# Performance work log

Measured on AMD Instinct MI355X. Metric: run time of the kernel, lower is better.

Reference implementation:

```python
import jax, jax.numpy as jnp
import numpy as np

DIM = 128      # transformer_dim = bottleneck_ch
NHEADS = 4
NEXP = 16
EHID = 256
WS = 8         # window_size
EPS = 1e-5     # LayerNorm eps


def setup_inputs() -> dict:
    key = jax.random.key(0)
    ks = jax.random.split(key, 6)
    B, H, W = 2, 128, 128
    N = H * W
    s = 0.02
    return {
        "x": jax.random.normal(ks[0], (B, N, DIM), jnp.float32),
        "ln1_g": jnp.ones((DIM,), jnp.float32),
        "ln1_b": jnp.zeros((DIM,), jnp.float32),
        "w_qkv": jax.random.normal(ks[1], (3 * DIM, DIM), jnp.float32) * s,
        "b_qkv": jnp.zeros((3 * DIM,), jnp.float32),
        "w_proj": jax.random.normal(ks[2], (DIM, DIM), jnp.float32) * s,
        "b_proj": jnp.zeros((DIM,), jnp.float32),
        "ln2_g": jnp.ones((DIM,), jnp.float32),
        "ln2_b": jnp.zeros((DIM,), jnp.float32),
        "gate_w": jax.random.normal(ks[3], (NEXP, DIM), jnp.float32) * s,
        "w1": jax.random.normal(ks[4], (NEXP, EHID, DIM), jnp.float32) * s,
        "b1": jnp.zeros((NEXP, EHID), jnp.float32),
        "w2": jax.random.normal(ks[5], (NEXP, DIM, EHID), jnp.float32) * s,
        "b2": jnp.zeros((NEXP, DIM), jnp.float32),
        "H": H,
        "W": W,
    }


def _ln(x, g, b):
    m = jnp.mean(x, axis=-1, keepdims=True)
    v = jnp.var(x, axis=-1, keepdims=True)
    return (x - m) * jax.lax.rsqrt(v + EPS) * g + b


def _win_attn(x, H, W, w_qkv, b_qkv, w_proj, b_proj):
    # x: (B, N, C); H,W divisible by WS (no padding branch needed)
    B, N, C = x.shape
    hd = C // NHEADS
    nH, nW = H // WS, W // WS
    # window partition: (B, N, C) -> (B*nH*nW, WS*WS, C)
    xw = x.reshape(B, nH, WS, nW, WS, C).transpose(0, 1, 3, 2, 4, 5)
    xw = xw.reshape(B * nH * nW, WS * WS, C)
    qkv = xw @ w_qkv.T + b_qkv
    q, k, v = jnp.split(qkv, 3, axis=-1)
    def heads(t):
        return t.reshape(-1, WS * WS, NHEADS, hd).transpose(0, 2, 1, 3)
    q, k, v = heads(q), heads(k), heads(v)
    scores = jnp.einsum('whqd,whkd->whqk', q, k) / jnp.sqrt(jnp.float32(hd))
    a = jax.nn.softmax(scores, axis=-1)
    o = jnp.einsum('whqk,whkd->whqd', a, v).transpose(0, 2, 1, 3)
    o = o.reshape(-1, WS * WS, C) @ w_proj.T + b_proj
    # window merge back to (B, N, C)
    o = o.reshape(B, nH, nW, WS, WS, C).transpose(0, 1, 3, 2, 4, 5)
    return o.reshape(B, N, C)


def _moe(x, gate_w, w1, b1, w2, b2):
    # top_k = 1 routing, eval mode (no noise / aux losses)
    B, N, C = x.shape
    f = x.reshape(-1, C)                      # (T, C)
    logits = f @ gate_w.T                     # (T, E)
    probs = jax.nn.softmax(logits, axis=-1)
    p = jnp.max(probs, axis=-1)               # top-1 prob
    idx = jnp.argmax(probs, axis=-1)          # top-1 expert id
    wgt = p / (p + 1e-8)                      # top_k_probs / (sum + eps)
    out = jnp.zeros_like(f)
    for e in range(NEXP):                     # small fixed expert loop
        h = jax.nn.gelu(f @ w1[e].T + b1[e], approximate=False)
        eo = h @ w2[e].T + b2[e]
        out = out + jnp.where((idx == e)[:, None], eo, 0.0)
    return (out * wgt[:, None]).reshape(B, N, C)


def reference(x, ln1_g, ln1_b, w_qkv, b_qkv, w_proj, b_proj,
              ln2_g, ln2_b, gate_w, w1, b1, w2, b2, H, W):
    x = x + _win_attn(_ln(x, ln1_g, ln1_b), H, W, w_qkv, b_qkv, w_proj, b_proj)
    x = x + _moe(_ln(x, ln2_g, ln2_b), gate_w, w1, b1, w2, b2)
    return x
```

## Files before the change

### kernel.cpp

```cpp
#include <hip/hip_runtime.h>
#include <math.h>

#define T_TOK 32768
#define DIM 128
#define NHEADS 4
#define HD 32
#define NEXP 16
#define EHID 256
#define NWIN 512
#define EPS 1e-5f
#define CPAD 16
#define XFS 132

typedef _Float16 f16x8 __attribute__((ext_vector_type(8)));
typedef _Float16 f16x4 __attribute__((ext_vector_type(4)));
typedef float f32x4v __attribute__((ext_vector_type(4)));

#define MFMA16(a, b, c) __builtin_amdgcn_mfma_f32_16x16x32_f16(a, b, c, 0, 0, 0)
#define LO_SCALE 4096.0f
#define LO_INV (1.0f / 4096.0f)

__device__ __forceinline__ int sw128(int r, int c) {
    return r * 128 + (((c >> 3) ^ (r & 7)) << 3) + (c & 7);
}
__device__ __forceinline__ int sw64(int r, int c) {
    return r * 64 + (((c >> 3) ^ (r & 7)) << 3) + (c & 7);
}
__device__ __forceinline__ int sw64p(int r, int c) {
    return r * 64 + (((c >> 3) ^ ((r ^ (r >> 3)) & 7)) << 3) + (c & 7);
}
__device__ __forceinline__ int swht(int tok, int hid) {
    return tok * 256 + (((hid >> 3) ^ (tok & 7)) << 3) + (hid & 7);
}

__global__ __launch_bounds__(256) void k_cvt(
    const float* __restrict__ wqkv, const float* __restrict__ wproj,
    _Float16* __restrict__ wq_h, _Float16* __restrict__ wq_l,
    _Float16* __restrict__ wp_h, _Float16* __restrict__ wp_l,
    int* __restrict__ counts)
{
    int i = blockIdx.x * 256 + threadIdx.x;
    if (blockIdx.x == 0 && threadIdx.x < NEXP * CPAD) counts[threadIdx.x] = 0;
    if (i < 3 * DIM * DIM / 4) {
        float4 f = ((const float4*)wqkv)[i];
        float fv[4] = {f.x, f.y, f.z, f.w};
        f16x4 h, l;
        #pragma unroll
        for (int j = 0; j < 4; ++j) {
            _Float16 hh = (_Float16)fv[j];
            h[j] = hh;
            l[j] = (_Float16)((fv[j] - (float)hh) * LO_SCALE);
        }
        *(f16x4*)(wq_h + (size_t)i * 4) = h;
        *(f16x4*)(wq_l + (size_t)i * 4) = l;
    }
    if (i < DIM * DIM / 4) {
        float4 f = ((const float4*)wproj)[i];
        float fv[4] = {f.x, f.y, f.z, f.w};
        f16x4 h, l;
        #pragma unroll
        for (int j = 0; j < 4; ++j) {
            _Float16 hh = (_Float16)fv[j];
            h[j] = hh;
            l[j] = (_Float16)((fv[j] - (float)hh) * LO_SCALE);
        }
        *(f16x4*)(wp_h + (size_t)i * 4) = h;
        *(f16x4*)(wp_l + (size_t)i * 4) = l;
    }
}

__global__ __launch_bounds__(1024) void k_attn(
    const float* __restrict__ x,
    const float* __restrict__ ln_g, const float* __restrict__ ln_b,
    const _Float16* __restrict__ wq_h, const _Float16* __restrict__ wq_l,
    const float* __restrict__ b_qkv,
    const _Float16* __restrict__ wp_h, const _Float16* __restrict__ wp_l,
    const float* __restrict__ b_proj,
    const float* __restrict__ ln2_g, const float* __restrict__ ln2_b,
    const float* __restrict__ gw,
    const float* __restrict__ w1, const float* __restrict__ w2,
    _Float16* __restrict__ w1h, _Float16* __restrict__ w2h,
    float* __restrict__ x2, _Float16* __restrict__ y2,
    float* __restrict__ wgt, int* __restrict__ perm, int* __restrict__ counts)
{
    __shared__ __align__(16) char smem[131072];
    _Float16* xoh = (_Float16*)(smem);
    _Float16* xol = (_Float16*)(smem + 16384);
    _Float16* qh  = (_Float16*)(smem + 32768);
    _Float16* ql  = (_Float16*)(smem + 49152);
    _Float16* kh  = (_Float16*)(smem + 65536);
    _Float16* kl  = (_Float16*)(smem + 81920);
    _Float16* vth = (_Float16*)(smem + 98304);
    _Float16* vtl = (_Float16*)(smem + 114688);
    float* xf   = (float*)(smem + 32768);
    float* ylds = (float*)(smem + 66560);
    float* lgs  = (float*)(smem + 99584);

    int tid = threadIdx.x;
    int w = tid >> 6, lane = tid & 63;
    int l15 = lane & 15, lg = lane >> 4;
    int wid = blockIdx.x;
    int wb = wid >> 8, wrr = (wid >> 4) & 15, wcc = wid & 15;
    const int tokbase = wb * 16384 + wrr * 1024 + wcc * 8;
    const size_t base = (size_t)tokbase * DIM;

    f16x8 qbh[2][4], qbl[2][4];
    float qbias[2];
    #pragma unroll
    for (int tl = 0; tl < 2; ++tl) {
        if (tl == 1 && w >= 8) break;
        int o = ((tl == 0) ? w : 16 + w) * 16 + l15;
        qbias[tl] = b_qkv[o];
        #pragma unroll
        for (int ks = 0; ks < 4; ++ks) {
            size_t wo = (size_t)o * DIM + ks * 32 + lg * 8;
            qbh[tl][ks] = *(const f16x8*)(wq_h + wo);
            qbl[tl][ks] = *(const f16x8*)(wq_l + wo);
        }
    }
    float xres[8];
    {
        int rt = w & 3, cb = (w >> 2) * 32;
        #pragma unroll
        for (int ct = 0; ct < 2; ++ct) {
            int c = cb + ct * 16 + l15;
            #pragma unroll
            for (int r = 0; r < 4; ++r) {
                int q = rt * 16 + lg * 4 + r;
                xres[ct * 4 + r] = x[base + (size_t)(q >> 3) * 16384 + (size_t)(q & 7) * DIM + c];
            }
        }
    }

    {
        int tt = tid >> 4, sub = tid & 15;
        const float* xr = x + base + (size_t)(tt >> 3) * 16384 + (size_t)(tt & 7) * DIM + sub * 8;
        float v[8];
        float s = 0.f, sq = 0.f;
        #pragma unroll
        for (int j = 0; j < 2; ++j) {
            float4 t4 = *(const float4*)(xr + j * 4);
            v[4 * j] = t4.x; v[4 * j + 1] = t4.y; v[4 * j + 2] = t4.z; v[4 * j + 3] = t4.w;
            s += (t4.x + t4.y) + (t4.z + t4.w);
            sq = fmaf(t4.x, t4.x, fmaf(t4.y, t4.y, fmaf(t4.z, t4.z, fmaf(t4.w, t4.w, sq))));
        }
        s += __shfl_xor(s, 1); sq += __shfl_xor(sq, 1);
        s += __shfl_xor(s, 2); sq += __shfl_xor(sq, 2);
        s += __shfl_xor(s, 4); sq += __shfl_xor(sq, 4);
        s += __shfl_xor(s, 8); sq += __shfl_xor(sq, 8);
        float m = s * (1.f / DIM);
        float var = sq * (1.f / DIM) - m * m;
        float rs = rsqrtf(var + EPS);
        _Float16 hh[8], ll[8];
        #pragma unroll
        for (int j = 0; j < 8; ++j) {
            int k = sub * 8 + j;
            float a = (v[j] - m) * rs * ln_g[k] + ln_b[k];
            _Float16 h = (_Float16)a;
            hh[j] = h;
            ll[j] = (_Float16)((a - (float)h) * LO_SCALE);
        }
        *(f16x8*)&xoh[sw128(tt, sub * 8)] = *(const f16x8*)&hh[0];
        *(f16x8*)&xol[sw128(tt, sub * 8)] = *(const f16x8*)&ll[0];
    }
    __syncthreads();

    #pragma unroll
    for (int tl = 0; tl < 2; ++tl) {
        if (tl == 1 && w >= 8) break;
        int o = ((tl == 0) ? w : 16 + w) * 16 + l15;
        f32x4v am[4], ac[4];
        #pragma unroll
        for (int rt = 0; rt < 4; ++rt) { am[rt] = 0.0f; ac[rt] = 0.0f; }
        #pragma unroll
        for (int rt = 0; rt < 4; ++rt) {
            #pragma unroll
            for (int ks = 0; ks < 4; ++ks) {
                f16x8 ah = *(const f16x8*)&xoh[sw128(rt * 16 + l15, ks * 32 + lg * 8)];
                f16x8 al = *(const f16x8*)&xol[sw128(rt * 16 + l15, ks * 32 + lg * 8)];
                am[rt] = MFMA16(ah, qbh[tl][ks], am[rt]);
                ac[rt] = MFMA16(ah, qbl[tl][ks], ac[rt]);
                ac[rt] = MFMA16(al, qbh[tl][ks], ac[rt]);
            }
        }
        float bias = qbias[tl];
        if (o < 256) {
            #pragma unroll
            for (int rt = 0; rt < 4; ++rt) {
                #pragma unroll
                for (int r = 0; r < 4; ++r) {
                    int row = rt * 16 + lg * 4 + r;
                    float val = am[rt][r] + ac[rt][r] * LO_INV + bias;
                    _Float16 h = (_Float16)val;
                    _Float16 lo = (_Float16)((val - (float)h) * LO_SCALE);
                    if (o < 128) { qh[sw128(row, o)] = h;       ql[sw128(row, o)] = lo; }
                    else         { kh[sw128(row, o - 128)] = h; kl[sw128(row, o - 128)] = lo; }
                }
            }
        } else {
            int d = o - 256;
            #pragma unroll
            for (int rt = 0; rt < 4; ++rt) {
                f16x4 vh4, vl4;
                #pragma unroll
                for (int r = 0; r < 4; ++r) {
                    float val = am[rt][r] + ac[rt][r] * LO_INV + bias;
                    _Float16 h = (_Float16)val;
                    vh4[r] = h;
                    vl4[r] = (_Float16)((val - (float)h) * LO_SCALE);
                }
                int tok0 = rt * 16 + lg * 4;
                *(f16x4*)&vth[sw64(d, tok0)] = vh4;
                *(f16x4*)&vtl[sw64(d, tok0)] = vl4;
            }
        }
    }
    __syncthreads();

    const float scale = 0.17677669529663687f;
    int h = w & 3;
    int qo = h * HD, rg = w >> 2;
    float preg[4][4];
    {
        f16x8 kbh[4], kbl[4];
        #pragma unroll
        for (int ct = 0; ct < 4; ++ct) {
            kbh[ct] = *(const f16x8*)&kh[sw128(ct * 16 + l15, qo + lg * 8)];
            kbl[ct] = *(const f16x8*)&kl[sw128(ct * 16 + l15, qo + lg * 8)];
        }
        f16x8 qah = *(const f16x8*)&qh[sw128(rg * 16 + l15, qo + lg * 8)];
        f16x8 qal = *(const f16x8*)&ql[sw128(rg * 16 + l15, qo + lg * 8)];
        f32x4v sm[4], sc2[4];
        #pragma unroll
        for (int ct = 0; ct < 4; ++ct) {
            sm[ct] = 0.0f; sc2[ct] = 0.0f;
            sm[ct] = MFMA16(qah, kbh[ct], sm[ct]);
            sc2[ct] = MFMA16(qah, kbl[ct], sc2[ct]);
            sc2[ct] = MFMA16(qal, kbh[ct], sc2[ct]);
        }
        #pragma unroll
        for (int r = 0; r < 4; ++r) {
            float v0 = (sm[0][r] + sc2[0][r] * LO_INV) * scale;
            float v1 = (sm[1][r] + sc2[1][r] * LO_INV) * scale;
            float v2 = (sm[2][r] + sc2[2][r] * LO_INV) * scale;
            float v3 = (sm[3][r] + sc2[3][r] * LO_INV) * scale;
            float mx = fmaxf(fmaxf(v0, v1), fmaxf(v2, v3));
            mx = fmaxf(mx, __shfl_xor(mx, 1));
            mx = fmaxf(mx, __shfl_xor(mx, 2));
            mx = fmaxf(mx, __shfl_xor(mx, 4));
            mx = fmaxf(mx, __shfl_xor(mx, 8));
            float e0 = expf(v0 - mx), e1 = expf(v1 - mx), e2 = expf(v2 - mx), e3 = expf(v3 - mx);
            float ss = (e0 + e1) + (e2 + e3);
            ss += __shfl_xor(ss, 1); ss += __shfl_xor(ss, 2);
            ss += __shfl_xor(ss, 4); ss += __shfl_xor(ss, 8);
            float inv = 1.f / ss;
            preg[0][r] = e0 * inv;
            preg[1][r] = e1 * inv;
            preg[2][r] = e2 * inv;
            preg[3][r] = e3 * inv;
        }
    }
    __syncthreads();

    {
        _Float16* dsth = (h < 2) ? qh : kh;
        _Float16* dstl = (h < 2) ? ql : kl;
        int pb = (h & 1) * 4096;
        #pragma unroll
        for (int ct = 0; ct < 4; ++ct) {
            #pragma unroll
            for (int r = 0; r < 4; ++r) {
                float p = preg[ct][r];
                int row = rg * 16 + lg * 4 + r, col = ct * 16 + l15;
                _Float16 hh = (_Float16)p;
                dsth[pb + sw64p(row, col)] = hh;
                dstl[pb + sw64p(row, col)] = (_Float16)((p - (float)hh) * LO_SCALE);
            }
        }
    }

    {
        const _Float16* psh = (h < 2) ? qh : kh;
        const _Float16* psl = (h < 2) ? ql : kl;
        int pb = (h & 1) * 4096;
        f16x8 vbh[2][2], vbl[2][2];
        #pragma unroll
        for (int ks = 0; ks < 2; ++ks)
            #pragma unroll
            for (int ct = 0; ct < 2; ++ct) {
                vbh[ks][ct] = *(const f16x8*)&vth[sw64(qo + ct * 16 + l15, ks * 32 + lg * 8)];
                vbl[ks][ct] = *(const f16x8*)&vtl[sw64(qo + ct * 16 + l15, ks * 32 + lg * 8)];
            }
        f32x4v om[2], oc[2];
        om[0] = 0.0f; om[1] = 0.0f; oc[0] = 0.0f; oc[1] = 0.0f;
        #pragma unroll
        for (int ks = 0; ks < 2; ++ks) {
            f16x8 pah = *(const f16x8*)&psh[pb + sw64p(rg * 16 + l15, ks * 32 + lg * 8)];
            f16x8 pal = *(const f16x8*)&psl[pb + sw64p(rg * 16 + l15, ks * 32 + lg * 8)];
            #pragma unroll
            for (int ct = 0; ct < 2; ++ct) {
                om[ct] = MFMA16(pah, vbh[ks][ct], om[ct]);
                oc[ct] = MFMA16(pah, vbl[ks][ct], oc[ct]);
                oc[ct] = MFMA16(pal, vbh[ks][ct], oc[ct]);
            }
        }
        #pragma unroll
        for (int ct = 0; ct < 2; ++ct) {
            #pragma unroll
            for (int r = 0; r < 4; ++r) {
                float val = om[ct][r] + oc[ct][r] * LO_INV;
                int row = rg * 16 + lg * 4 + r, col = qo + ct * 16 + l15;
                _Float16 hh = (_Float16)val;
                xoh[sw128(row, col)] = hh;
                xol[sw128(row, col)] = (_Float16)((val - (float)hh) * LO_SCALE);
            }
        }
    }

    f16x8 wpbh[2][4], wpbl[2][4];
    float pbias[2];
    {
        int cb = (w >> 2) * 32;
        #pragma unroll
        for (int ct = 0; ct < 2; ++ct) {
            int c = cb + ct * 16 + l15;
            pbias[ct] = b_proj[c];
            #pragma unroll
            for (int ks = 0; ks < 4; ++ks) {
                wpbh[ct][ks] = *(const f16x8*)(wp_h + (size_t)c * DIM + ks * 32 + lg * 8);
                wpbl[ct][ks] = *(const f16x8*)(wp_l + (size_t)c * DIM + ks * 32 + lg * 8);
            }
        }
    }
    __syncthreads();

    {
        int rt = w & 3, cb = (w >> 2) * 32;
        f32x4v pm[2], pc[2];
        pm[0] = 0.0f; pm[1] = 0.0f; pc[0] = 0.0f; pc[1] = 0.0f;
        #pragma unroll
        for (int ks = 0; ks < 4; ++ks) {
            f16x8 ah = *(const f16x8*)&xoh[sw128(rt * 16 + l15, ks * 32 + lg * 8)];
            f16x8 al = *(const f16x8*)&xol[sw128(rt * 16 + l15, ks * 32 + lg * 8)];
            #pragma unroll
            for (int ct = 0; ct < 2; ++ct) {
                pm[ct] = MFMA16(ah, wpbh[ct][ks], pm[ct]);
                pc[ct] = MFMA16(ah, wpbl[ct][ks], pc[ct]);
                pc[ct] = MFMA16(al, wpbh[ct][ks], pc[ct]);
            }
        }
        #pragma unroll
        for (int ct = 0; ct < 2; ++ct) {
            int c = cb + ct * 16 + l15;
            #pragma unroll
            for (int r = 0; r < 4; ++r) {
                int q = rt * 16 + lg * 4 + r;
                xf[q * XFS + c] = xres[ct * 4 + r] + (pm[ct][r] + pc[ct][r] * LO_INV + pbias[ct]);
            }
        }
    }
    __syncthreads();

    float vrow[8];
    _Float16 yh[8];
    {
        int tt = tid >> 4, sub = tid & 15;
        const float* xr = xf + tt * XFS + sub * 8;
        float s = 0.f, sq = 0.f;
        #pragma unroll
        for (int j = 0; j < 8; ++j) {
            float t = xr[j];
            vrow[j] = t;
            s += t;
            sq = fmaf(t, t, sq);
        }
        s += __shfl_xor(s, 1); sq += __shfl_xor(sq, 1);
        s += __shfl_xor(s, 2); sq += __shfl_xor(sq, 2);
        s += __shfl_xor(s, 4); sq += __shfl_xor(sq, 4);
        s += __shfl_xor(s, 8); sq += __shfl_xor(sq, 8);
        float m = s * (1.f / DIM);
        float var = sq * (1.f / DIM) - m * m;
        float rs = rsqrtf(var + EPS);
        #pragma unroll
        for (int j = 0; j < 8; ++j) {
            int k = sub * 8 + j;
            float a = (vrow[j] - m) * rs * ln2_g[k] + ln2_b[k];
            ylds[tt * 129 + k] = a;
            yh[j] = (_Float16)a;
        }
    }
    __syncthreads();

    {
        int tk = tid & 63, eg = tid >> 6;
        const float* g0 = gw + eg * DIM;
        float a0 = 0.f, a1 = 0.f, a2 = 0.f, a3 = 0.f;
        #pragma unroll 4
        for (int k = 0; k < DIM; k += 4) {
            a0 = fmaf(ylds[tk * 129 + k],     g0[k],     a0);
            a1 = fmaf(ylds[tk * 129 + k + 1], g0[k + 1], a1);
            a2 = fmaf(ylds[tk * 129 + k + 2], g0[k + 2], a2);
            a3 = fmaf(ylds[tk * 129 + k + 3], g0[k + 3], a3);
        }
        lgs[tk * 20 + eg] = (a0 + a1) + (a2 + a3);
    }
    __syncthreads();

    if (tid < 64) {
        float mx = -1e30f; int am = 0;
        #pragma unroll
        for (int e = 0; e < NEXP; ++e) {
            float v = lgs[tid * 20 + e];
            if (v > mx) { mx = v; am = e; }
        }
        float ss = 0.f;
        #pragma unroll
        for (int e = 0; e < NEXP; ++e) ss += expf(lgs[tid * 20 + e] - mx);
        float p = 1.f / ss;
        int gtok = tokbase + (tid >> 3) * 128 + (tid & 7);
        wgt[gtok] = p / (p + 1e-8f);

        int myrank = 0, mycnt = 0;
        #pragma unroll
        for (int e = 0; e < NEXP; ++e) {
            unsigned long long mask = __ballot(am == e);
            if (am == e) myrank = (int)__popcll(mask & ((1ull << tid) - 1));
            if (tid == e) mycnt = (int)__popcll(mask);
        }
        int bky = 0;
        if (tid < NEXP) bky = atomicAdd(&counts[tid * CPAD], mycnt);
        bky = __shfl(bky, am);
        perm[(size_t)am * T_TOK + bky + myrank] = gtok;
    }

    if (tid >= 64 && tid < 320) {
        int idx = wid * 256 + (tid - 64);
        float4 a = ((const float4*)w1)[idx];
        f16x4 h;
        h[0] = (_Float16)a.x; h[1] = (_Float16)a.y; h[2] = (_Float16)a.z; h[3] = (_Float16)a.w;
        *(f16x4*)(w1h + (size_t)idx * 4) = h;
        float4 b = ((const float4*)w2)[idx];
        f16x4 h2;
        h2[0] = (_Float16)b.x; h2[1] = (_Float16)b.y; h2[2] = (_Float16)b.z; h2[3] = (_Float16)b.w;
        *(f16x4*)(w2h + (size_t)idx * 4) = h2;
    }

    {
        int tt = tid >> 4, sub = tid & 15;
        int gtok = tokbase + (tt >> 3) * 128 + (tt & 7);
        float4* dst = (float4*)(x2 + (size_t)gtok * DIM + sub * 8);
        dst[0] = make_float4(vrow[0], vrow[1], vrow[2], vrow[3]);
        dst[1] = make_float4(vrow[4], vrow[5], vrow[6], vrow[7]);
        *(f16x8*)(y2 + (size_t)gtok * DIM + sub * 8) = *(const f16x8*)&yh[0];
    }
}

__global__ __launch_bounds__(256, 3) void k_expert(
    const _Float16* __restrict__ y2, const float* __restrict__ x2,
    const _Float16* __restrict__ w1h, const float* __restrict__ b1,
    const _Float16* __restrict__ w2h, const float* __restrict__ b2,
    const int* __restrict__ perm, const int* __restrict__ counts,
    const float* __restrict__ wgt, float* __restrict__ out)
{
    __shared__ _Float16 yt[64 * 128];
    __shared__ _Float16 ht[64 * 256];
    __shared__ int rows[64];

    int bflat = blockIdx.x;
    int e = -1, tile = 0, acc0 = 0;
    #pragma unroll
    for (int ee = 0; ee < NEXP; ++ee) {
        int t = (counts[ee * CPAD] + 63) >> 6;
        if (e < 0 && bflat < acc0 + t) { e = ee; tile = bflat - acc0; }
        acc0 += t;
    }
    if (e < 0) return;
    int cnt = counts[e * CPAD];
    int row0 = tile << 6;
    int nr = min(64, cnt - row0);
    int tid = threadIdx.x, wv = tid >> 6, lane = tid & 63;
    int l15 = lane & 15, lg = lane >> 4;

    if (tid < 64) rows[tid] = (tid < nr) ? perm[(size_t)e * T_TOK + row0 + tid] : 0;
    __syncthreads();
    f16x8 vz = (_Float16)0.0f;
    for (int i = tid; i < 1024; i += 256) {
        int tt = i >> 4, k = (i & 15) * 8;
        f16x8 val = vz;
        if (tt < nr) val = *(const f16x8*)(y2 + (size_t)rows[tt] * DIM + k);
        *(f16x8*)&yt[sw128(tt, k)] = val;
    }
    __syncthreads();

    {
        f16x8 yb[4][4];
        #pragma unroll
        for (int ct = 0; ct < 4; ++ct)
            #pragma unroll
            for (int ks = 0; ks < 4; ++ks)
                yb[ct][ks] = *(const f16x8*)&yt[sw128(ct * 16 + l15, ks * 32 + lg * 8)];
        #pragma unroll
        for (int rt = 0; rt < 4; ++rt) {
            int hid_row = wv * 64 + rt * 16 + l15;
            f16x8 a1[4];
            #pragma unroll
            for (int ks = 0; ks < 4; ++ks)
                a1[ks] = *(const f16x8*)(w1h + ((size_t)e * EHID + hid_row) * DIM + ks * 32 + lg * 8);
            f32x4v acc[4];
            #pragma unroll
            for (int ct = 0; ct < 4; ++ct) acc[ct] = 0.0f;
            #pragma unroll
            for (int ct = 0; ct < 4; ++ct)
                #pragma unroll
                for (int ks = 0; ks < 4; ++ks)
                    acc[ct] = MFMA16(a1[ks], yb[ct][ks], acc[ct]);
            int hid0 = wv * 64 + rt * 16 + lg * 4;
            float4 bb4 = *(const float4*)(b1 + e * EHID + hid0);
            float bbv[4] = {bb4.x, bb4.y, bb4.z, bb4.w};
            #pragma unroll
            for (int ct = 0; ct < 4; ++ct) {
                f16x4 hv;
                #pragma unroll
                for (int r = 0; r < 4; ++r) {
                    float a = acc[ct][r] + bbv[r];
                    float gl = 0.5f * a * (1.f + erff(a * 0.70710678118654752f));
                    hv[r] = (_Float16)gl;
                }
                int tok = ct * 16 + l15;
                *(f16x4*)&ht[swht(tok, hid0)] = hv;
            }
        }
    }
    __syncthreads();

    {
        f16x8 wb[2][8];
        #pragma unroll
        for (int ct = 0; ct < 2; ++ct) {
            int c = wv * 32 + ct * 16 + l15;
            #pragma unroll
            for (int ks = 0; ks < 8; ++ks)
                wb[ct][ks] = *(const f16x8*)(w2h + ((size_t)e * DIM + c) * EHID + ks * 32 + lg * 8);
        }
        #pragma unroll
        for (int rt = 0; rt < 4; ++rt) {
            f16x8 af[8];
            #pragma unroll
            for (int ks = 0; ks < 8; ++ks)
                af[ks] = *(const f16x8*)&ht[swht(rt * 16 + l15, ks * 32 + lg * 8)];
            f32x4v acc2[2];
            acc2[0] = 0.0f; acc2[1] = 0.0f;
            #pragma unroll
            for (int ks = 0; ks < 8; ++ks)
                #pragma unroll
                for (int ct = 0; ct < 2; ++ct)
                    acc2[ct] = MFMA16(af[ks], wb[ct][ks], acc2[ct]);
            #pragma unroll
            for (int ct = 0; ct < 2; ++ct) {
                int c = wv * 32 + ct * 16 + l15;
                float bb = b2[e * DIM + c];
                #pragma unroll
                for (int r = 0; r < 4; ++r) {
                    int tt = rt * 16 + lg * 4 + r;
                    if (tt < nr) {
                        int gtok = rows[tt];
                        size_t go = (size_t)gtok * DIM + c;
                        out[go] = x2[go] + wgt[gtok] * (acc2[ct][r] + bb);
                    }
                }
            }
        }
    }
}

extern "C" void kernel_launch(void* const* d_in, const int* in_sizes, int n_in,
                              void* d_out, int out_size, void* d_ws, size_t ws_size,
                              hipStream_t stream) {
    const float* x      = (const float*)d_in[0];
    const float* ln1_g  = (const float*)d_in[1];
    const float* ln1_b  = (const float*)d_in[2];
    const float* w_qkv  = (const float*)d_in[3];
    const float* b_qkv  = (const float*)d_in[4];
    const float* w_proj = (const float*)d_in[5];
    const float* b_proj = (const float*)d_in[6];
    const float* ln2_g  = (const float*)d_in[7];
    const float* ln2_b  = (const float*)d_in[8];
    const float* gate_w = (const float*)d_in[9];
    const float* w1     = (const float*)d_in[10];
    const float* b1     = (const float*)d_in[11];
    const float* w2     = (const float*)d_in[12];
    const float* b2     = (const float*)d_in[13];
    float* out = (float*)d_out;

    char* p = (char*)d_ws;
    float* x2 = (float*)p;                 p += (size_t)T_TOK * DIM * 4;
    _Float16* y2 = (_Float16*)p;           p += (size_t)T_TOK * DIM * 2;
    _Float16* wq_h = (_Float16*)p;         p += 3 * DIM * DIM * 2;
    _Float16* wq_l = (_Float16*)p;         p += 3 * DIM * DIM * 2;
    _Float16* wp_h = (_Float16*)p;         p += DIM * DIM * 2;
    _Float16* wp_l = (_Float16*)p;         p += DIM * DIM * 2;
    _Float16* w1h = (_Float16*)p;          p += NEXP * EHID * DIM * 2;
    _Float16* w2h = (_Float16*)p;          p += NEXP * EHID * DIM * 2;
    float* wgt = (float*)p;                p += T_TOK * 4;
    int* perm = (int*)p;                   p += (size_t)NEXP * T_TOK * 4;
    int* counts = (int*)p;                 p += NEXP * CPAD * 4;

    k_cvt<<<48, 256, 0, stream>>>(w_qkv, w_proj, wq_h, wq_l, wp_h, wp_l, counts);
    k_attn<<<NWIN, 1024, 0, stream>>>(x, ln1_g, ln1_b, wq_h, wq_l, b_qkv,
                                      wp_h, wp_l, b_proj, ln2_g, ln2_b, gate_w,
                                      w1, w2, w1h, w2h,
                                      x2, y2, wgt, perm, counts);
    k_expert<<<544, 256, 0, stream>>>(y2, x2, w1h, b1, w2h, b2, perm, counts, wgt, out);
}
```

Measured before the change: 105.6 us.

## Drop split-fp16 low parts in QKV and attention, fold LN2 into gate weights

Removes the low-order fp16 correction terms for the QKV weights, Q/K/V, scores and probabilities, so each of those matmuls uses one or two MFMAs where it used three, and only the high-part LDS buffers remain. Shared memory per block shrinks from 128 KB to 80 KB, which may allow higher occupancy. Gate logits are now computed from the raw residual rows by folding the LN2 gain and bias into precomputed gate weights and per-expert sums, so the LN2 output no longer has to be stored in LDS as fp32. The cost is lower precision in attention, which could change top-1 expert routing for tokens near a tie.

```diff
diff --git a/kernel.cpp b/kernel.cpp
--- a/kernel.cpp
+++ b/kernel.cpp
@@ -10,7 +10,7 @@
 #define NWIN 512
 #define EPS 1e-5f
 #define CPAD 16
-#define XFS 132
+#define XFS 133
 
 typedef _Float16 f16x8 __attribute__((ext_vector_type(8)));
 typedef _Float16 f16x4 __attribute__((ext_vector_type(4)));
@@ -35,14 +35,23 @@
 
 __global__ __launch_bounds__(256) void k_cvt(
     const float* __restrict__ wqkv, const float* __restrict__ wproj,
-    _Float16* __restrict__ wq_h, _Float16* __restrict__ wq_l,
+    const float* __restrict__ gw, const float* __restrict__ ln2_g,
+    const float* __restrict__ ln2_b,
+    _Float16* __restrict__ wq_h,
     _Float16* __restrict__ wp_h, _Float16* __restrict__ wp_l,
+    float* __restrict__ gw2, float* __restrict__ SA,
     int* __restrict__ counts)
 {
     int i = blockIdx.x * 256 + threadIdx.x;
     if (blockIdx.x == 0 && threadIdx.x < NEXP * CPAD) counts[threadIdx.x] = 0;
     if (i < 3 * DIM * DIM / 4) {
         float4 f = ((const float4*)wqkv)[i];
+        f16x4 h;
+        h[0] = (_Float16)f.x; h[1] = (_Float16)f.y; h[2] = (_Float16)f.z; h[3] = (_Float16)f.w;
+        *(f16x4*)(wq_h + (size_t)i * 4) = h;
+    }
+    if (i < DIM * DIM / 4) {
+        float4 f = ((const float4*)wproj)[i];
         float fv[4] = {f.x, f.y, f.z, f.w};
         f16x4 h, l;
         #pragma unroll
@@ -51,50 +60,48 @@
             h[j] = hh;
             l[j] = (_Float16)((fv[j] - (float)hh) * LO_SCALE);
         }
-        *(f16x4*)(wq_h + (size_t)i * 4) = h;
-        *(f16x4*)(wq_l + (size_t)i * 4) = l;
-    }
-    if (i < DIM * DIM / 4) {
-        float4 f = ((const float4*)wproj)[i];
-        float fv[4] = {f.x, f.y, f.z, f.w};
-        f16x4 h, l;
-        #pragma unroll
-        for (int j = 0; j < 4; ++j) {
-            _Float16 hh = (_Float16)fv[j];
-            h[j] = hh;
-            l[j] = (_Float16)((fv[j] - (float)hh) * LO_SCALE);
-        }
         *(f16x4*)(wp_h + (size_t)i * 4) = h;
         *(f16x4*)(wp_l + (size_t)i * 4) = l;
     }
-}
-
-__global__ __launch_bounds__(1024) void k_attn(
+    if (i < NEXP * DIM) {
+        int k = i & 127;
+        gw2[i] = ln2_g[k] * gw[i];
+    }
+    if (blockIdx.x == 1 && threadIdx.x < 2 * NEXP) {
+        int e = threadIdx.x >> 1;
+        const float* gr = gw + e * DIM;
+        float s = 0.f;
+        if (threadIdx.x & 1) {
+            for (int k = 0; k < DIM; ++k) s = fmaf(ln2_b[k], gr[k], s);
+        } else {
+            for (int k = 0; k < DIM; ++k) s = fmaf(ln2_g[k], gr[k], s);
+        }
+        SA[threadIdx.x] = s;
+    }
+}
+
+__global__ __launch_bounds__(1024, 8) void k_attn(
     const float* __restrict__ x,
     const float* __restrict__ ln_g, const float* __restrict__ ln_b,
-    const _Float16* __restrict__ wq_h, const _Float16* __restrict__ wq_l,
-    const float* __restrict__ b_qkv,
+    const _Float16* __restrict__ wq_h, const float* __restrict__ b_qkv,
     const _Float16* __restrict__ wp_h, const _Float16* __restrict__ wp_l,
     const float* __restrict__ b_proj,
     const float* __restrict__ ln2_g, const float* __restrict__ ln2_b,
-    const float* __restrict__ gw,
+    const float* __restrict__ gw2, const float* __restrict__ SA,
     const float* __restrict__ w1, const float* __restrict__ w2,
     _Float16* __restrict__ w1h, _Float16* __restrict__ w2h,
     float* __restrict__ x2, _Float16* __restrict__ y2,
     float* __restrict__ wgt, int* __restrict__ perm, int* __restrict__ counts)
 {
-    __shared__ __align__(16) char smem[131072];
+    __shared__ __align__(16) char smem[81920];
     _Float16* xoh = (_Float16*)(smem);
     _Float16* xol = (_Float16*)(smem + 16384);
     _Float16* qh  = (_Float16*)(smem + 32768);
-    _Float16* ql  = (_Float16*)(smem + 49152);
-    _Float16* kh  = (_Float16*)(smem + 65536);
-    _Float16* kl  = (_Float16*)(smem + 81920);
-    _Float16* vth = (_Float16*)(smem + 98304);
-    _Float16* vtl = (_Float16*)(smem + 114688);
-    float* xf   = (float*)(smem + 32768);
-    float* ylds = (float*)(smem + 66560);
-    float* lgs  = (float*)(smem + 99584);
+    _Float16* kh  = (_Float16*)(smem + 49152);
+    _Float16* vth = (_Float16*)(smem + 65536);
+    float* xf  = (float*)(smem + 32768);
+    float* mrs = (float*)(smem + 67072);
+    float* lgs = (float*)(smem + 67840);
 
     int tid = threadIdx.x;
     int w = tid >> 6, lane = tid & 63;
@@ -104,7 +111,7 @@
     const int tokbase = wb * 16384 + wrr * 1024 + wcc * 8;
     const size_t base = (size_t)tokbase * DIM;
 
-    f16x8 qbh[2][4], qbl[2][4];
+    f16x8 qbh[2][4];
     float qbias[2];
     #pragma unroll
     for (int tl = 0; tl < 2; ++tl) {
@@ -112,11 +119,8 @@
         int o = ((tl == 0) ? w : 16 + w) * 16 + l15;
         qbias[tl] = b_qkv[o];
         #pragma unroll
-        for (int ks = 0; ks < 4; ++ks) {
-            size_t wo = (size_t)o * DIM + ks * 32 + lg * 8;
-            qbh[tl][ks] = *(const f16x8*)(wq_h + wo);
-            qbl[tl][ks] = *(const f16x8*)(wq_l + wo);
-        }
+        for (int ks = 0; ks < 4; ++ks)
+            qbh[tl][ks] = *(const f16x8*)(wq_h + (size_t)o * DIM + ks * 32 + lg * 8);
     }
     float xres[8];
     {
@@ -179,7 +183,6 @@
                 f16x8 ah = *(const f16x8*)&xoh[sw128(rt * 16 + l15, ks * 32 + lg * 8)];
                 f16x8 al = *(const f16x8*)&xol[sw128(rt * 16 + l15, ks * 32 + lg * 8)];
                 am[rt] = MFMA16(ah, qbh[tl][ks], am[rt]);
-                ac[rt] = MFMA16(ah, qbl[tl][ks], ac[rt]);
                 ac[rt] = MFMA16(al, qbh[tl][ks], ac[rt]);
             }
         }
@@ -192,26 +195,19 @@
                     int row = rt * 16 + lg * 4 + r;
                     float val = am[rt][r] + ac[rt][r] * LO_INV + bias;
                     _Float16 h = (_Float16)val;
-                    _Float16 lo = (_Float16)((val - (float)h) * LO_SCALE);
-                    if (o < 128) { qh[sw128(row, o)] = h;       ql[sw128(row, o)] = lo; }
-                    else         { kh[sw128(row, o - 128)] = h; kl[sw128(row, o - 128)] = lo; }
+                    if (o < 128) qh[sw128(row, o)] = h;
+                    else         kh[sw128(row, o - 128)] = h;
                 }
             }
         } else {
             int d = o - 256;
             #pragma unroll
             for (int rt = 0; rt < 4; ++rt) {
-                f16x4 vh4, vl4;
+                f16x4 vh4;
                 #pragma unroll
-                for (int r = 0; r < 4; ++r) {
-                    float val = am[rt][r] + ac[rt][r] * LO_INV + bias;
-                    _Float16 h = (_Float16)val;
-                    vh4[r] = h;
-                    vl4[r] = (_Float16)((val - (float)h) * LO_SCALE);
-                }
-                int tok0 = rt * 16 + lg * 4;
-                *(f16x4*)&vth[sw64(d, tok0)] = vh4;
-                *(f16x4*)&vtl[sw64(d, tok0)] = vl4;
+                for (int r = 0; r < 4; ++r)
+                    vh4[r] = (_Float16)(am[rt][r] + ac[rt][r] * LO_INV + bias);
+                *(f16x4*)&vth[sw64(d, rt * 16 + lg * 4)] = vh4;
             }
         }
     }
@@ -222,28 +218,23 @@
     int qo = h * HD, rg = w >> 2;
     float preg[4][4];
     {
-        f16x8 kbh[4], kbl[4];
+        f16x8 kbh[4];
+        #pragma unroll
+        for (int ct = 0; ct < 4; ++ct)
+            kbh[ct] = *(const f16x8*)&kh[sw128(ct * 16 + l15, qo + lg * 8)];
+        f16x8 qah = *(const f16x8*)&qh[sw128(rg * 16 + l15, qo + lg * 8)];
+        f32x4v sm[4];
         #pragma unroll
         for (int ct = 0; ct < 4; ++ct) {
-            kbh[ct] = *(const f16x8*)&kh[sw128(ct * 16 + l15, qo + lg * 8)];
-            kbl[ct] = *(const f16x8*)&kl[sw128(ct * 16 + l15, qo + lg * 8)];
-        }
-        f16x8 qah = *(const f16x8*)&qh[sw128(rg * 16 + l15, qo + lg * 8)];
-        f16x8 qal = *(const f16x8*)&ql[sw128(rg * 16 + l15, qo + lg * 8)];
-        f32x4v sm[4], sc2[4];
-        #pragma unroll
-        for (int ct = 0; ct < 4; ++ct) {
-            sm[ct] = 0.0f; sc2[ct] = 0.0f;
+            sm[ct] = 0.0f;
             sm[ct] = MFMA16(qah, kbh[ct], sm[ct]);
-            sc2[ct] = MFMA16(qah, kbl[ct], sc2[ct]);
-            sc2[ct] = MFMA16(qal, kbh[ct], sc2[ct]);
         }
         #pragma unroll
         for (int r = 0; r < 4; ++r) {
-            float v0 = (sm[0][r] + sc2[0][r] * LO_INV) * scale;
-            float v1 = (sm[1][r] + sc2[1][r] * LO_INV) * scale;
-            float v2 = (sm[2][r] + sc2[2][r] * LO_INV) * scale;
-            float v3 = (sm[3][r] + sc2[3][r] * LO_INV) * scale;
+            float v0 = sm[0][r] * scale;
+            float v1 = sm[1][r] * scale;
+            float v2 = sm[2][r] * scale;
+            float v3 = sm[3][r] * scale;
             float mx = fmaxf(fmaxf(v0, v1), fmaxf(v2, v3));
             mx = fmaxf(mx, __shfl_xor(mx, 1));
             mx = fmaxf(mx, __shfl_xor(mx, 2));
@@ -264,51 +255,40 @@
 
     {
         _Float16* dsth = (h < 2) ? qh : kh;
-        _Float16* dstl = (h < 2) ? ql : kl;
         int pb = (h & 1) * 4096;
         #pragma unroll
         for (int ct = 0; ct < 4; ++ct) {
             #pragma unroll
             for (int r = 0; r < 4; ++r) {
-                float p = preg[ct][r];
                 int row = rg * 16 + lg * 4 + r, col = ct * 16 + l15;
-                _Float16 hh = (_Float16)p;
-                dsth[pb + sw64p(row, col)] = hh;
-                dstl[pb + sw64p(row, col)] = (_Float16)((p - (float)hh) * LO_SCALE);
+                dsth[pb + sw64p(row, col)] = (_Float16)preg[ct][r];
             }
         }
     }
 
     {
         const _Float16* psh = (h < 2) ? qh : kh;
-        const _Float16* psl = (h < 2) ? ql : kl;
         int pb = (h & 1) * 4096;
-        f16x8 vbh[2][2], vbl[2][2];
+        f16x8 vbh[2][2];
         #pragma unroll
         for (int ks = 0; ks < 2; ++ks)
             #pragma unroll
-            for (int ct = 0; ct < 2; ++ct) {
+            for (int ct = 0; ct < 2; ++ct)
                 vbh[ks][ct] = *(const f16x8*)&vth[sw64(qo + ct * 16 + l15, ks * 32 + lg * 8)];
-                vbl[ks][ct] = *(const f16x8*)&vtl[sw64(qo + ct * 16 + l15, ks * 32 + lg * 8)];
-            }
-        f32x4v om[2], oc[2];
-        om[0] = 0.0f; om[1] = 0.0f; oc[0] = 0.0f; oc[1] = 0.0f;
+        f32x4v om[2];
+        om[0] = 0.0f; om[1] = 0.0f;
         #pragma unroll
         for (int ks = 0; ks < 2; ++ks) {
             f16x8 pah = *(const f16x8*)&psh[pb + sw64p(rg * 16 + l15, ks * 32 + lg * 8)];
-            f16x8 pal = *(const f16x8*)&psl[pb + sw64p(rg * 16 + l15, ks * 32 + lg * 8)];
-            #pragma unroll
-            for (int ct = 0; ct < 2; ++ct) {
+            #pragma unroll
+            for (int ct = 0; ct < 2; ++ct)
                 om[ct] = MFMA16(pah, vbh[ks][ct], om[ct]);
-                oc[ct] = MFMA16(pah, vbl[ks][ct], oc[ct]);
-                oc[ct] = MFMA16(pal, vbh[ks][ct], oc[ct]);
-            }
         }
         #pragma unroll
         for (int ct = 0; ct < 2; ++ct) {
             #pragma unroll
             for (int r = 0; r < 4; ++r) {
-                float val = om[ct][r] + oc[ct][r] * LO_INV;
+                float val = om[ct][r];
                 int row = rg * 16 + lg * 4 + r, col = qo + ct * 16 + l15;
                 _Float16 hh = (_Float16)val;
                 xoh[sw128(row, col)] = hh;
@@ -384,25 +364,28 @@
         #pragma unroll
         for (int j = 0; j < 8; ++j) {
             int k = sub * 8 + j;
-            float a = (vrow[j] - m) * rs * ln2_g[k] + ln2_b[k];
-            ylds[tt * 129 + k] = a;
-            yh[j] = (_Float16)a;
-        }
+            yh[j] = (_Float16)((vrow[j] - m) * rs * ln2_g[k] + ln2_b[k]);
+        }
+        if (sub == 0) { mrs[tt * 2] = m; mrs[tt * 2 + 1] = rs; }
     }
     __syncthreads();
 
     {
         int tk = tid & 63, eg = tid >> 6;
-        const float* g0 = gw + eg * DIM;
+        const float* g0 = gw2 + eg * DIM;
+        float S_e = SA[eg * 2], A_e = SA[eg * 2 + 1];
+        float m = mrs[tk * 2], rs = mrs[tk * 2 + 1];
+        const float* xr = xf + tk * XFS;
         float a0 = 0.f, a1 = 0.f, a2 = 0.f, a3 = 0.f;
         #pragma unroll 4
         for (int k = 0; k < DIM; k += 4) {
-            a0 = fmaf(ylds[tk * 129 + k],     g0[k],     a0);
-            a1 = fmaf(ylds[tk * 129 + k + 1], g0[k + 1], a1);
-            a2 = fmaf(ylds[tk * 129 + k + 2], g0[k + 2], a2);
-            a3 = fmaf(ylds[tk * 129 + k + 3], g0[k + 3], a3);
-        }
-        lgs[tk * 20 + eg] = (a0 + a1) + (a2 + a3);
+            a0 = fmaf(xr[k],     g0[k],     a0);
+            a1 = fmaf(xr[k + 1], g0[k + 1], a1);
+            a2 = fmaf(xr[k + 2], g0[k + 2], a2);
+            a3 = fmaf(xr[k + 3], g0[k + 3], a3);
+        }
+        float dot = (a0 + a1) + (a2 + a3);
+        lgs[tk * 20 + eg] = rs * (dot - m * S_e) + A_e;
     }
     __syncthreads();
 
@@ -596,18 +579,20 @@
     float* x2 = (float*)p;                 p += (size_t)T_TOK * DIM * 4;
     _Float16* y2 = (_Float16*)p;           p += (size_t)T_TOK * DIM * 2;
     _Float16* wq_h = (_Float16*)p;         p += 3 * DIM * DIM * 2;
-    _Float16* wq_l = (_Float16*)p;         p += 3 * DIM * DIM * 2;
     _Float16* wp_h = (_Float16*)p;         p += DIM * DIM * 2;
     _Float16* wp_l = (_Float16*)p;         p += DIM * DIM * 2;
     _Float16* w1h = (_Float16*)p;          p += NEXP * EHID * DIM * 2;
     _Float16* w2h = (_Float16*)p;          p += NEXP * EHID * DIM * 2;
+    float* gw2 = (float*)p;                p += NEXP * DIM * 4;
+    float* SA = (float*)p;                 p += 2 * NEXP * 4;
     float* wgt = (float*)p;                p += T_TOK * 4;
     int* perm = (int*)p;                   p += (size_t)NEXP * T_TOK * 4;
     int* counts = (int*)p;                 p += NEXP * CPAD * 4;
 
-    k_cvt<<<48, 256, 0, stream>>>(w_qkv, w_proj, wq_h, wq_l, wp_h, wp_l, counts);
-    k_attn<<<NWIN, 1024, 0, stream>>>(x, ln1_g, ln1_b, wq_h, wq_l, b_qkv,
-                                      wp_h, wp_l, b_proj, ln2_g, ln2_b, gate_w,
+    k_cvt<<<48, 256, 0, stream>>>(w_qkv, w_proj, gate_w, ln2_g, ln2_b,
+                                  wq_h, wp_h, wp_l, gw2, SA, counts);
+    k_attn<<<NWIN, 1024, 0, stream>>>(x, ln1_g, ln1_b, wq_h, b_qkv,
+                                      wp_h, wp_l, b_proj, ln2_g, ln2_b, gw2, SA,
                                       w1, w2, w1h, w2h,
                                       x2, y2, wgt, perm, counts);
     k_expert<<<544, 256, 0, stream>>>(y2, x2, w1h, b1, w2h, b2, perm, counts, wgt, out);
```

After: 121.8 us. +15.4%, slower.
